# Kernel optimization log

Measured on AMD Instinct MI355X. Metric: run time of the kernel, lower is better.

Reference implementation:

```python
import jax, jax.numpy as jnp
import numpy as np

B, N, D = 4, 2048, 1024
DC = 256
E = 8            # n_experts
TOPK = 2
EXP = 4
HID = EXP * D
CAPF = 1.25
T = B * N
CAP = int(CAPF * TOPK * T / E)  # static expert capacity (2560)
EPS = 1e-5


def _transition_adaln(x, cond, mask, Wada, bada, W1, b1, W2, b2):
    # adaLN-modulated gated MLP expert: x [..., D], cond [..., DC], mask [...]
    ada = cond @ Wada + bada                      # [..., 3D]
    shift, scale, gate = jnp.split(ada, 3, axis=-1)
    mu = jnp.mean(x, axis=-1, keepdims=True)
    var = jnp.mean(jnp.square(x - mu), axis=-1, keepdims=True)
    h = (x - mu) * jax.lax.rsqrt(var + EPS)       # LayerNorm, no affine
    h = h * (1.0 + scale) + shift
    h = jax.nn.gelu(h @ W1 + b1) @ W2 + b2
    return gate * h * mask[..., None]


def setup_inputs() -> dict:
    key = jax.random.key(0)
    ks = jax.random.split(key, 16)
    s = lambda k, shp, f: jax.random.normal(k, shp, jnp.float32) * f
    return {
        "x": s(ks[0], (B, N, D), 1.0),
        "cond": s(ks[1], (B, N, DC), 1.0),
        "mask": jnp.ones((B, N), jnp.float32),
        "Wg": s(ks[2], (D, E - 1), 0.02),
        # shared expert
        "Wada_s": s(ks[3], (DC, 3 * D), 0.02),
        "bada_s": jnp.zeros((3 * D,), jnp.float32),
        "W1_s": s(ks[4], (D, HID), 0.02),
        "b1_s": jnp.zeros((HID,), jnp.float32),
        "W2_s": s(ks[5], (HID, D), 0.02),
        "b2_s": jnp.zeros((D,), jnp.float32),
        # routed experts (stacked over E)
        "Wada_e": s(ks[6], (E, DC, 3 * D), 0.02),
        "bada_e": jnp.zeros((E, 3 * D), jnp.float32),
        "W1_e": s(ks[7], (E, D, HID), 0.02),
        "b1_e": jnp.zeros((E, HID), jnp.float32),
        "W2_e": s(ks[8], (E, HID, D), 0.02),
        "b2_e": jnp.zeros((E, D), jnp.float32),
    }


def reference(x, cond, mask, Wg, Wada_s, bada_s, W1_s, b1_s, W2_s, b2_s,
              Wada_e, bada_e, W1_e, b1_e, W2_e, b2_e):
    xf = x.reshape(T, D)
    cf = cond.reshape(T, DC)
    mf = mask.reshape(T)

    # --- router: softmax over E-1 experts, top-k, normalized weights ---
    scores = jax.nn.softmax(xf @ Wg, axis=-1)              # [T, E-1]
    w, idx = jax.lax.top_k(scores, TOPK)                   # [T, K]
    w = w / jnp.sum(w, axis=-1, keepdims=True)

    flat_e = idx.reshape(-1)                               # [T*K] expert ids
    flat_w = w.reshape(-1)

    # --- indices_and_bins: stable sort by expert, histogram, cumsum ---
    order = jnp.argsort(flat_e, stable=True)               # [T*K]
    tpe = jnp.bincount(flat_e, length=E)                   # tokens per expert
    starts = jnp.cumsum(tpe) - tpe                         # exclusive cumsum

    # --- binned gather into [E, CAP] slots (overflow dropped, pad zeros) ---
    slot = jnp.arange(CAP)
    pos = starts[:, None] + slot[None, :]                  # [E, CAP]
    valid = slot[None, :] < tpe[:, None]                   # [E, CAP]
    pos_c = jnp.clip(pos, 0, T * TOPK - 1)
    sidx = order[pos_c]                                    # sorted flat index
    tok = sidx // TOPK                                     # source token id
    vf = valid.astype(x.dtype)
    xg = xf[tok] * vf[..., None]                           # [E, CAP, D]
    cg = cf[tok] * vf[..., None]                           # [E, CAP, DC]
    mg = mf[tok] * vf                                      # [E, CAP]

    # --- per-expert grouped compute (vmapped over E) ---
    y = jax.vmap(_transition_adaln)(xg, cg, mg, Wada_e, bada_e,
                                    W1_e, b1_e, W2_e, b2_e)  # [E, CAP, D]

    # --- binned scatter with expert weights ---
    w_sel = flat_w[sidx] * vf                              # [E, CAP]
    contrib = (y * w_sel[..., None]).reshape(E * CAP, D)
    moe = jnp.zeros((T, D), x.dtype).at[tok.reshape(-1)].add(contrib)
    moe = moe.reshape(B, N, D)

    # --- shared expert + normalized combine ---
    x_shared = _transition_adaln(x, cond, mask, Wada_s, bada_s,
                                 W1_s, b1_s, W2_s, b2_s)
    return (x_shared + moe * TOPK) / (TOPK + 1)
```

## Files before the change

kernel.cpp:

```cpp
#include <hip/hip_runtime.h>
#include <cstdint>

#define B_    4
#define N_    2048
#define D_    1024
#define DC_   256
#define E_    8
#define NE    7
#define HID_  4096
#define T_    8192
#define CAP_  2560
#define TP_   16384

typedef unsigned short us;

__device__ __forceinline__ float b2f(us h) {
    unsigned u = ((unsigned)h) << 16; float f; __builtin_memcpy(&f, &u, 4); return f;
}
__device__ __forceinline__ us f2b(float f) {
    unsigned u; __builtin_memcpy(&u, &f, 4);
    unsigned r = (u + 0x7fffu + ((u >> 16) & 1u)) >> 16;
    return (us)r;
}

using short8 = __attribute__((ext_vector_type(8))) short;
using f32x4  = __attribute__((ext_vector_type(4))) float;

typedef __attribute__((address_space(1))) void GASV;
typedef __attribute__((address_space(3))) void LASV;
__device__ __forceinline__ void gld16(const void* g, void* l) {
    __builtin_amdgcn_global_load_lds((GASV*)g, (LASV*)l, 16, 0, 0);
}

__global__ void sentinel_kernel(float* out) { out[0] = 12345.0f; }

__global__ __launch_bounds__(256) void router_ln_kernel(
    const float* __restrict__ x, const float* __restrict__ Wg,
    int* __restrict__ flat_e, float* __restrict__ flat_w, us* __restrict__ lnb)
{
    __shared__ float sWg[D_ * NE];
    for (int i = threadIdx.x; i < D_ * NE; i += 256) sWg[i] = Wg[i];
    __syncthreads();
    const int wave = threadIdx.x >> 6, lane = threadIdx.x & 63;
    const int t = blockIdx.x * 4 + wave;
    const float* xr = x + (size_t)t * D_;

    float v[16];
#pragma unroll
    for (int q = 0; q < 4; q++) {
        float4 f = *(const float4*)(xr + lane * 16 + q * 4);
        v[q*4+0] = f.x; v[q*4+1] = f.y; v[q*4+2] = f.z; v[q*4+3] = f.w;
    }
    float s7[NE] = {0,0,0,0,0,0,0};
    float sum = 0.f, sq = 0.f;
#pragma unroll
    for (int u = 0; u < 16; u++) {
        float xv = v[u]; int d = lane * 16 + u;
        sum += xv; sq += xv * xv;
#pragma unroll
        for (int j = 0; j < NE; j++) s7[j] += xv * sWg[d * NE + j];
    }
#pragma unroll
    for (int off = 32; off; off >>= 1) {
        sum += __shfl_xor(sum, off, 64);
        sq  += __shfl_xor(sq,  off, 64);
#pragma unroll
        for (int j = 0; j < NE; j++) s7[j] += __shfl_xor(s7[j], off, 64);
    }
    const float mu  = sum * (1.f / D_);
    const float var = sq * (1.f / D_) - mu * mu;
    const float rs  = rsqrtf(var + 1e-5f);

    us* lr = lnb + (size_t)t * D_ + lane * 16;
#pragma unroll
    for (int half = 0; half < 2; half++) {
        union { us h[8]; uint4 u4; } p;
#pragma unroll
        for (int u = 0; u < 8; u++) p.h[u] = f2b((v[half*8+u] - mu) * rs);
        *(uint4*)(lr + half * 8) = p.u4;
    }
    if (lane == 0) {
        float m = s7[0];
#pragma unroll
        for (int j = 1; j < NE; j++) m = fmaxf(m, s7[j]);
        float ex[NE];
#pragma unroll
        for (int j = 0; j < NE; j++) ex[j] = __expf(s7[j] - m);
        int i1 = 0;
#pragma unroll
        for (int j = 1; j < NE; j++) if (ex[j] > ex[i1]) i1 = j;
        int i2 = (i1 == 0) ? 1 : 0;
#pragma unroll
        for (int j = 0; j < NE; j++) if (j != i1 && ex[j] > ex[i2]) i2 = j;
        float wA = ex[i1], wB = ex[i2], iw = 1.f / (wA + wB);
        flat_e[t*2]   = i1; flat_e[t*2+1] = i2;
        flat_w[t*2]   = wA * iw; flat_w[t*2+1] = wB * iw;
    }
}

__global__ __launch_bounds__(256) void binning_kernel(
    const int* __restrict__ flat_e, int* __restrict__ bin_idx,
    int* __restrict__ dest_slot, int* __restrict__ n_e)
{
    __shared__ int hist[NE][257];
    const int t = threadIdx.x;
    const int base = t * 64;
    int cnt[NE] = {0,0,0,0,0,0,0};
    for (int i = 0; i < 64; i++) {
        int fe = flat_e[base + i];
#pragma unroll
        for (int e = 0; e < NE; e++) cnt[e] += (fe == e);
    }
#pragma unroll
    for (int e = 0; e < NE; e++) hist[e][t] = cnt[e];
    __syncthreads();
    if (t < NE) {
        int run = 0;
        for (int i = 0; i < 256; i++) { int c = hist[t][i]; hist[t][i] = run; run += c; }
        n_e[t] = run < CAP_ ? run : CAP_;
    }
    __syncthreads();
    for (int i = t; i < NE * CAP_; i += 256) bin_idx[i] = -1;
    __syncthreads();
    int ofs[NE];
#pragma unroll
    for (int e = 0; e < NE; e++) ofs[e] = hist[e][t];
    for (int i = 0; i < 64; i++) {
        int idx = base + i;
        int fe = flat_e[idx];
        int r = 0;
#pragma unroll
        for (int e = 0; e < NE; e++) if (fe == e) r = ofs[e]++;
        int slot = (r < CAP_) ? (fe * CAP_ + r) : -1;
        dest_slot[idx] = slot;
        if (slot >= 0) bin_idx[slot] = idx;
    }
}

__global__ void cvt_bf16_kernel(const float* __restrict__ in, us* __restrict__ out, long n) {
    long i = ((long)blockIdx.x * 256 + threadIdx.x) * 4;
    if (i >= n) return;
    float4 f = *(const float4*)(in + i);
    union { us h[4]; uint2 u; } p;
    p.h[0] = f2b(f.x); p.h[1] = f2b(f.y); p.h[2] = f2b(f.z); p.h[3] = f2b(f.w);
    *(uint2*)(out + i) = p.u;
}

__global__ __launch_bounds__(256) void convT_kernel(
    const float* __restrict__ W, us* __restrict__ WT, int K, int N, long sW, long sWT)
{
    const float* Wp = W + (size_t)blockIdx.z * sW;
    us* WTp = WT + (size_t)blockIdx.z * sWT;
    __shared__ us tl[32][33];
    const int k0 = blockIdx.y * 32, n0 = blockIdx.x * 32;
    const int tx = threadIdx.x & 31, ty = threadIdx.x >> 5;
#pragma unroll
    for (int r = ty; r < 32; r += 8)
        tl[r][tx] = f2b(Wp[(size_t)(k0 + r) * N + n0 + tx]);
    __syncthreads();
#pragma unroll
    for (int r = ty; r < 32; r += 8)
        WTp[(size_t)(n0 + r) * K + k0 + tx] = tl[tx][r];
}

__global__ __launch_bounds__(256) void gather_cond_kernel(
    const us* __restrict__ cond_bf, const int* __restrict__ bin_idx, us* __restrict__ cond_g)
{
    const int row = blockIdx.x * 4 + (threadIdx.x >> 6);
    const int lane = threadIdx.x & 63;
    const int pi = bin_idx[row];
    uint2 val = {0u, 0u};
    if (pi >= 0) val = *(const uint2*)(cond_bf + (size_t)(pi >> 1) * DC_ + lane * 4);
    *(uint2*)(cond_g + (size_t)row * DC_ + lane * 4) = val;
}

struct GArgs {
    const us* A; const us* BT; const float* bias;
    us* out0; us* out1; us* out2;
    const us* gateP; const float* maskP; float* outF;
    int M, N, K, ldOut;
    long sA_e, sBT_e, sBias_e, sOut_e;
    const int* n_e;
    int epi;
};

__global__ __launch_bounds__(256) void gemm_bt(GArgs g) {
    const int e = blockIdx.z;
    int rows = g.M;
    if (g.n_e) { int ne = g.n_e[e]; if (ne < rows) rows = ne; }
    const int mbase = blockIdx.y * 128;
    if (mbase >= rows) return;
    const int nbase = blockIdx.x * 128;
    const us* A  = g.A  + (size_t)e * g.sA_e;
    const us* BT = g.BT + (size_t)e * g.sBT_e;
    const int K = g.K;

    __shared__ __align__(16) us sA[128 * 32];
    __shared__ __align__(16) us sB[128 * 32];

    const int tid = threadIdx.x;
    const int wave = tid >> 6, lane = tid & 63;
    const int wm = wave >> 1, wn = wave & 1;
    const int lrow = lane & 15, lq = lane >> 4;
    const int r0 = lane >> 2;
    const int cb = (lane & 3) * 8;

    const size_t aOff0 = (size_t)(mbase + wave * 16 + r0) * K + cb;
    const size_t aOff1 = aOff0 + (size_t)64 * K;
    const size_t bOff0 = (size_t)(nbase + wave * 16 + r0) * K + cb;
    const size_t bOff1 = bOff0 + (size_t)64 * K;

    f32x4 acc[4][4];
#pragma unroll
    for (int i = 0; i < 4; i++)
#pragma unroll
        for (int j = 0; j < 4; j++) acc[i][j] = (f32x4)0.0f;

    for (int k0 = 0; k0 < K; k0 += 32) {
        gld16(A + aOff0 + k0, &sA[wave * 512]);
        gld16(A + aOff1 + k0, &sA[(wave + 4) * 512]);
        gld16(BT + bOff0 + k0, &sB[wave * 512]);
        gld16(BT + bOff1 + k0, &sB[(wave + 4) * 512]);
        __syncthreads();
        short8 af[4], bf[4];
#pragma unroll
        for (int i = 0; i < 4; i++) {
            af[i] = *(const short8*)&sA[(wm * 64 + i * 16 + lrow) * 32 + lq * 8];
            bf[i] = *(const short8*)&sB[(wn * 64 + i * 16 + lrow) * 32 + lq * 8];
        }
#pragma unroll
        for (int i = 0; i < 4; i++)
#pragma unroll
            for (int j = 0; j < 4; j++)
                acc[i][j] = __builtin_amdgcn_mfma_f32_16x16x32_bf16(af[i], bf[j], acc[i][j], 0, 0, 0);
        __syncthreads();
    }

    const float* bias = g.bias + (size_t)e * g.sBias_e;
    float bv[4];
#pragma unroll
    for (int j = 0; j < 4; j++) bv[j] = bias[nbase + wn * 64 + j * 16 + lrow];

    if (g.epi == 0) {
        const int seg = nbase >> 10;
        us* ob = (seg == 0) ? g.out0 : (seg == 1) ? g.out1 : g.out2;
        ob += (size_t)e * g.sOut_e;
        const int coll = nbase - (seg << 10) + wn * 64 + lrow;
#pragma unroll
        for (int i = 0; i < 4; i++)
#pragma unroll
            for (int r = 0; r < 4; r++) {
                int row = mbase + wm * 64 + i * 16 + lq * 4 + r;
#pragma unroll
                for (int j = 0; j < 4; j++)
                    ob[(size_t)row * 1024 + coll + j * 16] = f2b(acc[i][j][r] + bv[j]);
            }
    } else if (g.epi == 1) {
        us* ob = g.out0 + (size_t)e * g.sOut_e;
#pragma unroll
        for (int i = 0; i < 4; i++)
#pragma unroll
            for (int r = 0; r < 4; r++) {
                int row = mbase + wm * 64 + i * 16 + lq * 4 + r;
#pragma unroll
                for (int j = 0; j < 4; j++) {
                    float v = acc[i][j][r] + bv[j];
                    float u = 0.7978845608028654f * (v + 0.044715f * v * v * v);
                    float exu = __expf(2.f * u);
                    float th = 1.f - 2.f / (exu + 1.f);
                    ob[(size_t)row * g.ldOut + nbase + wn * 64 + j * 16 + lrow] = f2b(0.5f * v * (1.f + th));
                }
            }
    } else if (g.epi == 2) {
        us* ob = g.out0 + (size_t)e * g.sOut_e;
#pragma unroll
        for (int i = 0; i < 4; i++)
#pragma unroll
            for (int r = 0; r < 4; r++) {
                int row = mbase + wm * 64 + i * 16 + lq * 4 + r;
#pragma unroll
                for (int j = 0; j < 4; j++)
                    ob[(size_t)row * g.ldOut + nbase + wn * 64 + j * 16 + lrow] = f2b(acc[i][j][r] + bv[j]);
            }
    } else {
        float* ob = g.outF;
#pragma unroll
        for (int i = 0; i < 4; i++)
#pragma unroll
            for (int r = 0; r < 4; r++) {
                int row = mbase + wm * 64 + i * 16 + lq * 4 + r;
                float mrow = g.maskP[row] * (1.f / 3.f);
#pragma unroll
                for (int j = 0; j < 4; j++) {
                    int col = nbase + wn * 64 + j * 16 + lrow;
                    float v = acc[i][j][r] + bv[j];
                    ob[(size_t)row * 1024 + col] = v * b2f(g.gateP[(size_t)row * 1024 + col]) * mrow;
                }
            }
    }
}

__global__ void modulate_s_kernel(const us* __restrict__ lnb, const us* __restrict__ shift,
                                  const us* __restrict__ scale, us* __restrict__ hmod)
{
    size_t i = ((size_t)blockIdx.x * 256 + threadIdx.x) * 4;
    uint2 l  = *(const uint2*)(lnb + i);
    uint2 sh = *(const uint2*)(shift + i);
    uint2 sc = *(const uint2*)(scale + i);
    const us* lp = (const us*)&l; const us* shp = (const us*)&sh; const us* scp = (const us*)&sc;
    union { us h[4]; uint2 u; } o;
#pragma unroll
    for (int u = 0; u < 4; u++)
        o.h[u] = f2b(b2f(lp[u]) * (1.f + b2f(scp[u])) + b2f(shp[u]));
    *(uint2*)(hmod + i) = o.u;
}

__global__ void modulate_g_kernel(const us* __restrict__ lnb, const us* __restrict__ shift_g,
                                  const us* __restrict__ scale_g, const int* __restrict__ bin_idx,
                                  us* __restrict__ hmod_g)
{
    const int slot = blockIdx.x;
    const int d = threadIdx.x * 4;
    const int pi = bin_idx[slot];
    float lv[4] = {0.f, 0.f, 0.f, 0.f};
    if (pi >= 0) {
        uint2 l = *(const uint2*)(lnb + (size_t)(pi >> 1) * D_ + d);
        const us* lp = (const us*)&l;
#pragma unroll
        for (int u = 0; u < 4; u++) lv[u] = b2f(lp[u]);
    }
    const size_t off = (size_t)slot * 1024 + d;
    uint2 sh = *(const uint2*)(shift_g + off);
    uint2 sc = *(const uint2*)(scale_g + off);
    const us* shp = (const us*)&sh; const us* scp = (const us*)&sc;
    union { us h[4]; uint2 u; } o;
#pragma unroll
    for (int u = 0; u < 4; u++)
        o.h[u] = f2b(lv[u] * (1.f + b2f(scp[u])) + b2f(shp[u]));
    *(uint2*)(hmod_g + off) = o.u;
}

__global__ void combine_kernel(const us* __restrict__ y_g, const us* __restrict__ gate_g,
                               const int* __restrict__ dest_slot, const float* __restrict__ flat_w,
                               const float* __restrict__ maskp, float* __restrict__ out)
{
    const int t = blockIdx.x;
    const int d = threadIdx.x * 4;
    const size_t o = (size_t)t * D_ + d;
    float acc[4] = {0.f, 0.f, 0.f, 0.f};
    const int s0 = dest_slot[2*t], s1 = dest_slot[2*t+1];
    const float w0 = flat_w[2*t] * (2.f / 3.f), w1 = flat_w[2*t+1] * (2.f / 3.f);
    if (s0 >= 0) {
        uint2 yg = *(const uint2*)(y_g + (size_t)s0 * D_ + d);
        uint2 gg = *(const uint2*)(gate_g + (size_t)s0 * D_ + d);
        const us* yp = (const us*)&yg; const us* gp = (const us*)&gg;
#pragma unroll
        for (int u = 0; u < 4; u++) acc[u] += w0 * b2f(gp[u]) * b2f(yp[u]);
    }
    if (s1 >= 0) {
        uint2 yg = *(const uint2*)(y_g + (size_t)s1 * D_ + d);
        uint2 gg = *(const uint2*)(gate_g + (size_t)s1 * D_ + d);
        const us* yp = (const us*)&yg; const us* gp = (const us*)&gg;
#pragma unroll
        for (int u = 0; u < 4; u++) acc[u] += w1 * b2f(gp[u]) * b2f(yp[u]);
    }
    const float mk = maskp[t];
    float4 cur = *(float4*)(out + o);
    cur.x += acc[0] * mk; cur.y += acc[1] * mk;
    cur.z += acc[2] * mk; cur.w += acc[3] * mk;
    *(float4*)(out + o) = cur;
}

extern "C" void kernel_launch(void* const* d_in, const int* in_sizes, int n_in,
                              void* d_out, int out_size, void* d_ws, size_t ws_size,
                              hipStream_t stream)
{
    const float* x      = (const float*)d_in[0];
    const float* cond   = (const float*)d_in[1];
    const float* maskp  = (const float*)d_in[2];
    const float* Wg     = (const float*)d_in[3];
    const float* Wada_s = (const float*)d_in[4];
    const float* bada_s = (const float*)d_in[5];
    const float* W1_s   = (const float*)d_in[6];
    const float* b1_s   = (const float*)d_in[7];
    const float* W2_s   = (const float*)d_in[8];
    const float* b2_s   = (const float*)d_in[9];
    const float* Wada_e = (const float*)d_in[10];
    const float* bada_e = (const float*)d_in[11];
    const float* W1_e   = (const float*)d_in[12];
    const float* b1_e   = (const float*)d_in[13];
    const float* W2_e   = (const float*)d_in[14];
    const float* b2_e   = (const float*)d_in[15];
    (void)in_sizes; (void)n_in; (void)out_size;
    float* out = (float*)d_out;

    char* p = (char*)d_ws;
    size_t off = 0;
    auto carve = [&](size_t bytes) -> void* {
        void* r = p + off; off = (off + bytes + 255) & ~(size_t)255; return r;
    };
    int*   flat_e   = (int*)carve((size_t)TP_ * 4);
    float* flat_w   = (float*)carve((size_t)TP_ * 4);
    int*   bin_idx  = (int*)carve((size_t)NE * CAP_ * 4);
    int*   dest_slot= (int*)carve((size_t)TP_ * 4);
    int*   d_ne     = (int*)carve(256);
    us*    cond_bf  = (us*)carve((size_t)T_ * DC_ * 2);
    us*    lnb      = (us*)carve((size_t)T_ * D_ * 2);
    us*    gate_s   = (us*)carve((size_t)T_ * D_ * 2);
    us*    gate_g   = (us*)carve((size_t)NE * CAP_ * D_ * 2);
    us*    y_g      = (us*)carve((size_t)NE * CAP_ * D_ * 2);

    char* A = p + off;
    const size_t ARENA_SZ = 103809024;
    us* hmod_s  = (us*)(A);
    us* wt_s    = (us*)(A + 16777216);
    us* t1_s    = (us*)(A + 25165824);
    us* shift_s = (us*)(A + 25165824);
    us* scale_s = (us*)(A + 41943040);
    us* hmod_gb = (us*)(A);
    us* wt_b    = (us*)(A + 15728640);
    us* t1_gb   = (us*)(A + 40894464);
    us* shift_gb= (us*)(A + 40894464);
    us* scale_gb= (us*)(A + 40894464 + 15728640);
    us* cond_gb = (us*)(A + 40894464 + 31457280);

    if (off + ARENA_SZ > ws_size) {
        sentinel_kernel<<<1, 1, 0, stream>>>(out);
        return;
    }

    router_ln_kernel<<<T_ / 4, 256, 0, stream>>>(x, Wg, flat_e, flat_w, lnb);
    binning_kernel<<<1, 256, 0, stream>>>(flat_e, bin_idx, dest_slot, d_ne);
    cvt_bf16_kernel<<<(T_ * DC_) / 1024, 256, 0, stream>>>(cond, cond_bf, (long)T_ * DC_);

    GArgs a;
    a.gateP = nullptr; a.maskP = nullptr; a.outF = nullptr;

    convT_kernel<<<dim3(96, 8, 1), 256, 0, stream>>>(Wada_s, wt_s, DC_, 3072, 0, 0);
    a.A = cond_bf; a.BT = wt_s; a.bias = bada_s;
    a.out0 = shift_s; a.out1 = scale_s; a.out2 = gate_s;
    a.M = T_; a.N = 3072; a.K = DC_; a.ldOut = 1024;
    a.sA_e = 0; a.sBT_e = 0; a.sBias_e = 0; a.sOut_e = 0;
    a.n_e = nullptr; a.epi = 0;
    gemm_bt<<<dim3(24, T_ / 128, 1), 256, 0, stream>>>(a);

    modulate_s_kernel<<<(T_ * D_) / 1024, 256, 0, stream>>>(lnb, shift_s, scale_s, hmod_s);

    convT_kernel<<<dim3(128, 32, 1), 256, 0, stream>>>(W1_s, wt_s, D_, HID_, 0, 0);
    a.A = hmod_s; a.BT = wt_s; a.bias = b1_s; a.out0 = t1_s;
    a.M = T_; a.N = HID_; a.K = D_; a.ldOut = HID_; a.epi = 1;
    gemm_bt<<<dim3(HID_ / 128, T_ / 128, 1), 256, 0, stream>>>(a);

    convT_kernel<<<dim3(32, 128, 1), 256, 0, stream>>>(W2_s, wt_s, HID_, D_, 0, 0);
    a.A = t1_s; a.BT = wt_s; a.bias = b2_s; a.out0 = nullptr;
    a.gateP = gate_s; a.maskP = maskp; a.outF = out;
    a.M = T_; a.N = D_; a.K = HID_; a.ldOut = D_; a.epi = 3;
    gemm_bt<<<dim3(D_ / 128, T_ / 128, 1), 256, 0, stream>>>(a);
    a.gateP = nullptr; a.maskP = nullptr; a.outF = nullptr;

    const int bstart[3] = {0, 3, 6};
    const int bcnt[3]   = {3, 3, 1};
    for (int b = 0; b < 3; b++) {
        const int eb = bstart[b], Bb = bcnt[b];
        gather_cond_kernel<<<Bb * CAP_ / 4, 256, 0, stream>>>(
            cond_bf, bin_idx + (size_t)eb * CAP_, cond_gb);

        convT_kernel<<<dim3(96, 8, Bb), 256, 0, stream>>>(
            Wada_e + (size_t)eb * DC_ * 3072, wt_b, DC_, 3072,
            (long)DC_ * 3072, (long)DC_ * 3072);
        a.A = cond_gb; a.BT = wt_b; a.bias = bada_e + (size_t)eb * 3072;
        a.out0 = shift_gb; a.out1 = scale_gb;
        a.out2 = gate_g + (size_t)eb * CAP_ * 1024;
        a.M = CAP_; a.N = 3072; a.K = DC_; a.ldOut = 1024;
        a.sA_e = (long)CAP_ * DC_; a.sBT_e = (long)3072 * DC_;
        a.sBias_e = 3072; a.sOut_e = (long)CAP_ * 1024;
        a.n_e = d_ne + eb; a.epi = 0;
        gemm_bt<<<dim3(24, CAP_ / 128, Bb), 256, 0, stream>>>(a);

        modulate_g_kernel<<<Bb * CAP_, 256, 0, stream>>>(
            lnb, shift_gb, scale_gb, bin_idx + (size_t)eb * CAP_, hmod_gb);

        convT_kernel<<<dim3(128, 32, Bb), 256, 0, stream>>>(
            W1_e + (size_t)eb * D_ * HID_, wt_b, D_, HID_,
            (long)D_ * HID_, (long)D_ * HID_);
        a.A = hmod_gb; a.BT = wt_b; a.bias = b1_e + (size_t)eb * HID_; a.out0 = t1_gb;
        a.M = CAP_; a.N = HID_; a.K = D_; a.ldOut = HID_;
        a.sA_e = (long)CAP_ * D_; a.sBT_e = (long)HID_ * D_;
        a.sBias_e = HID_; a.sOut_e = (long)CAP_ * HID_;
        a.epi = 1;
        gemm_bt<<<dim3(HID_ / 128, CAP_ / 128, Bb), 256, 0, stream>>>(a);

        convT_kernel<<<dim3(32, 128, Bb), 256, 0, stream>>>(
            W2_e + (size_t)eb * HID_ * D_, wt_b, HID_, D_,
            (long)HID_ * D_, (long)HID_ * D_);
        a.A = t1_gb; a.BT = wt_b; a.bias = b2_e + (size_t)eb * D_;
        a.out0 = y_g + (size_t)eb * CAP_ * 1024;
        a.M = CAP_; a.N = D_; a.K = HID_; a.ldOut = D_;
        a.sA_e = (long)CAP_ * HID_; a.sBT_e = (long)D_ * HID_;
        a.sBias_e = D_; a.sOut_e = (long)CAP_ * 1024;
        a.epi = 2;
        gemm_bt<<<dim3(D_ / 128, CAP_ / 128, Bb), 256, 0, stream>>>(a);
    }

    combine_kernel<<<T_, 256, 0, stream>>>(y_g, gate_g, dest_slot, flat_w, maskp, out);
}
```

Baseline: 1.412 ms.

## Widen GEMM K-tile with swizzled LDS, templatize epilogues, vectorize transpose, parallel-scan binning

```diff
diff --git a/kernel.cpp b/kernel.cpp
--- a/kernel.cpp
+++ b/kernel.cpp
@@ -103,6 +103,7 @@
     int* __restrict__ dest_slot, int* __restrict__ n_e)
 {
     __shared__ int hist[NE][257];
+    __shared__ int sc[2][256];
     const int t = threadIdx.x;
     const int base = t * 64;
     int cnt[NE] = {0,0,0,0,0,0,0};
@@ -114,12 +115,21 @@
 #pragma unroll
     for (int e = 0; e < NE; e++) hist[e][t] = cnt[e];
     __syncthreads();
-    if (t < NE) {
-        int run = 0;
-        for (int i = 0; i < 256; i++) { int c = hist[t][i]; hist[t][i] = run; run += c; }
-        n_e[t] = run < CAP_ ? run : CAP_;
-    }
-    __syncthreads();
+    for (int e = 0; e < NE; e++) {
+        sc[0][t] = hist[e][t];
+        __syncthreads();
+        int src = 0;
+        for (int o = 1; o < 256; o <<= 1) {
+            int v = sc[src][t] + ((t >= o) ? sc[src][t - o] : 0);
+            sc[src ^ 1][t] = v;
+            __syncthreads();
+            src ^= 1;
+        }
+        int incl = sc[src][t];
+        hist[e][t] = incl - cnt[e];
+        if (t == 255) n_e[e] = incl < CAP_ ? incl : CAP_;
+        __syncthreads();
+    }
     for (int i = t; i < NE * CAP_; i += 256) bin_idx[i] = -1;
     __syncthreads();
     int ofs[NE];
@@ -151,16 +161,27 @@
 {
     const float* Wp = W + (size_t)blockIdx.z * sW;
     us* WTp = WT + (size_t)blockIdx.z * sWT;
-    __shared__ us tl[32][33];
-    const int k0 = blockIdx.y * 32, n0 = blockIdx.x * 32;
-    const int tx = threadIdx.x & 31, ty = threadIdx.x >> 5;
-#pragma unroll
-    for (int r = ty; r < 32; r += 8)
-        tl[r][tx] = f2b(Wp[(size_t)(k0 + r) * N + n0 + tx]);
+    __shared__ us tl[64][72];
+    const int k0 = blockIdx.y * 64, n0 = blockIdx.x * 64;
+    const int lr = threadIdx.x >> 4;
+    const int lc = threadIdx.x & 15;
+#pragma unroll
+    for (int p = 0; p < 4; p++) {
+        int r = p * 16 + lr;
+        float4 f = *(const float4*)(Wp + (size_t)(k0 + r) * N + n0 + lc * 4);
+        tl[lc*4+0][r] = f2b(f.x);
+        tl[lc*4+1][r] = f2b(f.y);
+        tl[lc*4+2][r] = f2b(f.z);
+        tl[lc*4+3][r] = f2b(f.w);
+    }
     __syncthreads();
-#pragma unroll
-    for (int r = ty; r < 32; r += 8)
-        WTp[(size_t)(n0 + r) * K + k0 + tx] = tl[tx][r];
+    const int nr = threadIdx.x >> 2, kc = (threadIdx.x & 3) * 16;
+    union { us h[16]; uint4 u4[2]; } pk;
+#pragma unroll
+    for (int u = 0; u < 16; u++) pk.h[u] = tl[nr][kc + u];
+    us* dst = WTp + (size_t)(n0 + nr) * K + k0 + kc;
+    *(uint4*)(dst) = pk.u4[0];
+    *(uint4*)(dst + 8) = pk.u4[1];
 }
 
 __global__ __launch_bounds__(256) void gather_cond_kernel(
@@ -181,58 +202,71 @@
     int M, N, K, ldOut;
     long sA_e, sBT_e, sBias_e, sOut_e;
     const int* n_e;
-    int epi;
 };
 
+template<int TN, int EPI>
 __global__ __launch_bounds__(256) void gemm_bt(GArgs g) {
     const int e = blockIdx.z;
     int rows = g.M;
     if (g.n_e) { int ne = g.n_e[e]; if (ne < rows) rows = ne; }
     const int mbase = blockIdx.y * 128;
     if (mbase >= rows) return;
-    const int nbase = blockIdx.x * 128;
-    const us* A  = g.A  + (size_t)e * g.sA_e;
-    const us* BT = g.BT + (size_t)e * g.sBT_e;
+    const int nbase = blockIdx.x * TN;
+    const us* Ap = g.A  + (size_t)e * g.sA_e;
+    const us* BTp = g.BT + (size_t)e * g.sBT_e;
     const int K = g.K;
 
-    __shared__ __align__(16) us sA[128 * 32];
-    __shared__ __align__(16) us sB[128 * 32];
+    constexpr int MI = (TN == 128) ? 4 : 2;
+    __shared__ __align__(16) us sA[128 * 64];
+    __shared__ __align__(16) us sB[TN * 64];
 
     const int tid = threadIdx.x;
     const int wave = tid >> 6, lane = tid & 63;
-    const int wm = wave >> 1, wn = wave & 1;
+    const int wm = (TN == 128) ? (wave >> 1) : wave;
+    const int wn = (TN == 128) ? (wave & 1) : 0;
     const int lrow = lane & 15, lq = lane >> 4;
-    const int r0 = lane >> 2;
-    const int cb = (lane & 3) * 8;
-
-    const size_t aOff0 = (size_t)(mbase + wave * 16 + r0) * K + cb;
-    const size_t aOff1 = aOff0 + (size_t)64 * K;
-    const size_t bOff0 = (size_t)(nbase + wave * 16 + r0) * K + cb;
-    const size_t bOff1 = bOff0 + (size_t)64 * K;
-
-    f32x4 acc[4][4];
-#pragma unroll
-    for (int i = 0; i < 4; i++)
+    const int rl = lane >> 3;
+    const int cs = (lane & 7) ^ rl;
+
+    f32x4 acc[MI][4];
+#pragma unroll
+    for (int i = 0; i < MI; i++)
 #pragma unroll
         for (int j = 0; j < 4; j++) acc[i][j] = (f32x4)0.0f;
 
-    for (int k0 = 0; k0 < K; k0 += 32) {
-        gld16(A + aOff0 + k0, &sA[wave * 512]);
-        gld16(A + aOff1 + k0, &sA[(wave + 4) * 512]);
-        gld16(BT + bOff0 + k0, &sB[wave * 512]);
-        gld16(BT + bOff1 + k0, &sB[(wave + 4) * 512]);
+    for (int k0 = 0; k0 < K; k0 += 64) {
+#pragma unroll
+        for (int q = 0; q < 4; q++) {
+            int row = wave * 32 + q * 8 + rl;
+            gld16(Ap + (size_t)(mbase + row) * K + k0 + cs * 8, &sA[(wave * 32 + q * 8) * 64]);
+        }
+#pragma unroll
+        for (int q = 0; q < TN / 32; q++) {
+            int row = wave * (TN / 4) + q * 8 + rl;
+            gld16(BTp + (size_t)(nbase + row) * K + k0 + cs * 8, &sB[(wave * (TN / 4) + q * 8) * 64]);
+        }
         __syncthreads();
-        short8 af[4], bf[4];
-#pragma unroll
-        for (int i = 0; i < 4; i++) {
-            af[i] = *(const short8*)&sA[(wm * 64 + i * 16 + lrow) * 32 + lq * 8];
-            bf[i] = *(const short8*)&sB[(wn * 64 + i * 16 + lrow) * 32 + lq * 8];
+#pragma unroll
+        for (int step = 0; step < 2; step++) {
+            short8 af[MI], bf[4];
+#pragma unroll
+            for (int i = 0; i < MI; i++) {
+                int r = wm * (MI * 16) + i * 16 + lrow;
+                int slot = (step * 4 + lq) ^ (r & 7);
+                af[i] = *(const short8*)&sA[r * 64 + slot * 8];
+            }
+#pragma unroll
+            for (int j = 0; j < 4; j++) {
+                int r = wn * 64 + j * 16 + lrow;
+                int slot = (step * 4 + lq) ^ (r & 7);
+                bf[j] = *(const short8*)&sB[r * 64 + slot * 8];
+            }
+#pragma unroll
+            for (int i = 0; i < MI; i++)
+#pragma unroll
+                for (int j = 0; j < 4; j++)
+                    acc[i][j] = __builtin_amdgcn_mfma_f32_16x16x32_bf16(af[i], bf[j], acc[i][j], 0, 0, 0);
         }
-#pragma unroll
-        for (int i = 0; i < 4; i++)
-#pragma unroll
-            for (int j = 0; j < 4; j++)
-                acc[i][j] = __builtin_amdgcn_mfma_f32_16x16x32_bf16(af[i], bf[j], acc[i][j], 0, 0, 0);
         __syncthreads();
     }
 
@@ -241,27 +275,27 @@
 #pragma unroll
     for (int j = 0; j < 4; j++) bv[j] = bias[nbase + wn * 64 + j * 16 + lrow];
 
-    if (g.epi == 0) {
+    if constexpr (EPI == 0) {
         const int seg = nbase >> 10;
         us* ob = (seg == 0) ? g.out0 : (seg == 1) ? g.out1 : g.out2;
         ob += (size_t)e * g.sOut_e;
         const int coll = nbase - (seg << 10) + wn * 64 + lrow;
 #pragma unroll
-        for (int i = 0; i < 4; i++)
+        for (int i = 0; i < MI; i++)
 #pragma unroll
             for (int r = 0; r < 4; r++) {
-                int row = mbase + wm * 64 + i * 16 + lq * 4 + r;
+                int row = mbase + wm * (MI * 16) + i * 16 + lq * 4 + r;
 #pragma unroll
                 for (int j = 0; j < 4; j++)
                     ob[(size_t)row * 1024 + coll + j * 16] = f2b(acc[i][j][r] + bv[j]);
             }
-    } else if (g.epi == 1) {
+    } else if constexpr (EPI == 1) {
         us* ob = g.out0 + (size_t)e * g.sOut_e;
 #pragma unroll
-        for (int i = 0; i < 4; i++)
+        for (int i = 0; i < MI; i++)
 #pragma unroll
             for (int r = 0; r < 4; r++) {
-                int row = mbase + wm * 64 + i * 16 + lq * 4 + r;
+                int row = mbase + wm * (MI * 16) + i * 16 + lq * 4 + r;
 #pragma unroll
                 for (int j = 0; j < 4; j++) {
                     float v = acc[i][j][r] + bv[j];
@@ -271,13 +305,13 @@
                     ob[(size_t)row * g.ldOut + nbase + wn * 64 + j * 16 + lrow] = f2b(0.5f * v * (1.f + th));
                 }
             }
-    } else if (g.epi == 2) {
+    } else if constexpr (EPI == 2) {
         us* ob = g.out0 + (size_t)e * g.sOut_e;
 #pragma unroll
-        for (int i = 0; i < 4; i++)
+        for (int i = 0; i < MI; i++)
 #pragma unroll
             for (int r = 0; r < 4; r++) {
-                int row = mbase + wm * 64 + i * 16 + lq * 4 + r;
+                int row = mbase + wm * (MI * 16) + i * 16 + lq * 4 + r;
 #pragma unroll
                 for (int j = 0; j < 4; j++)
                     ob[(size_t)row * g.ldOut + nbase + wn * 64 + j * 16 + lrow] = f2b(acc[i][j][r] + bv[j]);
@@ -285,10 +319,10 @@
     } else {
         float* ob = g.outF;
 #pragma unroll
-        for (int i = 0; i < 4; i++)
+        for (int i = 0; i < MI; i++)
 #pragma unroll
             for (int r = 0; r < 4; r++) {
-                int row = mbase + wm * 64 + i * 16 + lq * 4 + r;
+                int row = mbase + wm * (MI * 16) + i * 16 + lq * 4 + r;
                 float mrow = g.maskP[row] * (1.f / 3.f);
 #pragma unroll
                 for (int j = 0; j < 4; j++) {
@@ -436,26 +470,26 @@
     GArgs a;
     a.gateP = nullptr; a.maskP = nullptr; a.outF = nullptr;
 
-    convT_kernel<<<dim3(96, 8, 1), 256, 0, stream>>>(Wada_s, wt_s, DC_, 3072, 0, 0);
+    convT_kernel<<<dim3(48, 4, 1), 256, 0, stream>>>(Wada_s, wt_s, DC_, 3072, 0, 0);
     a.A = cond_bf; a.BT = wt_s; a.bias = bada_s;
     a.out0 = shift_s; a.out1 = scale_s; a.out2 = gate_s;
     a.M = T_; a.N = 3072; a.K = DC_; a.ldOut = 1024;
     a.sA_e = 0; a.sBT_e = 0; a.sBias_e = 0; a.sOut_e = 0;
-    a.n_e = nullptr; a.epi = 0;
-    gemm_bt<<<dim3(24, T_ / 128, 1), 256, 0, stream>>>(a);
+    a.n_e = nullptr;
+    gemm_bt<128, 0><<<dim3(24, T_ / 128, 1), 256, 0, stream>>>(a);
 
     modulate_s_kernel<<<(T_ * D_) / 1024, 256, 0, stream>>>(lnb, shift_s, scale_s, hmod_s);
 
-    convT_kernel<<<dim3(128, 32, 1), 256, 0, stream>>>(W1_s, wt_s, D_, HID_, 0, 0);
+    convT_kernel<<<dim3(64, 16, 1), 256, 0, stream>>>(W1_s, wt_s, D_, HID_, 0, 0);
     a.A = hmod_s; a.BT = wt_s; a.bias = b1_s; a.out0 = t1_s;
-    a.M = T_; a.N = HID_; a.K = D_; a.ldOut = HID_; a.epi = 1;
-    gemm_bt<<<dim3(HID_ / 128, T_ / 128, 1), 256, 0, stream>>>(a);
-
-    convT_kernel<<<dim3(32, 128, 1), 256, 0, stream>>>(W2_s, wt_s, HID_, D_, 0, 0);
+    a.M = T_; a.N = HID_; a.K = D_; a.ldOut = HID_;
+    gemm_bt<128, 1><<<dim3(HID_ / 128, T_ / 128, 1), 256, 0, stream>>>(a);
+
+    convT_kernel<<<dim3(16, 64, 1), 256, 0, stream>>>(W2_s, wt_s, HID_, D_, 0, 0);
     a.A = t1_s; a.BT = wt_s; a.bias = b2_s; a.out0 = nullptr;
     a.gateP = gate_s; a.maskP = maskp; a.outF = out;
-    a.M = T_; a.N = D_; a.K = HID_; a.ldOut = D_; a.epi = 3;
-    gemm_bt<<<dim3(D_ / 128, T_ / 128, 1), 256, 0, stream>>>(a);
+    a.M = T_; a.N = D_; a.K = HID_; a.ldOut = D_;
+    gemm_bt<64, 3><<<dim3(D_ / 64, T_ / 128, 1), 256, 0, stream>>>(a);
     a.gateP = nullptr; a.maskP = nullptr; a.outF = nullptr;
 
     const int bstart[3] = {0, 3, 6};
@@ -465,7 +499,7 @@
         gather_cond_kernel<<<Bb * CAP_ / 4, 256, 0, stream>>>(
             cond_bf, bin_idx + (size_t)eb * CAP_, cond_gb);
 
-        convT_kernel<<<dim3(96, 8, Bb), 256, 0, stream>>>(
+        convT_kernel<<<dim3(48, 4, Bb), 256, 0, stream>>>(
             Wada_e + (size_t)eb * DC_ * 3072, wt_b, DC_, 3072,
             (long)DC_ * 3072, (long)DC_ * 3072);
         a.A = cond_gb; a.BT = wt_b; a.bias = bada_e + (size_t)eb * 3072;
@@ -474,23 +508,22 @@
         a.M = CAP_; a.N = 3072; a.K = DC_; a.ldOut = 1024;
         a.sA_e = (long)CAP_ * DC_; a.sBT_e = (long)3072 * DC_;
         a.sBias_e = 3072; a.sOut_e = (long)CAP_ * 1024;
-        a.n_e = d_ne + eb; a.epi = 0;
-        gemm_bt<<<dim3(24, CAP_ / 128, Bb), 256, 0, stream>>>(a);
+        a.n_e = d_ne + eb;
+        gemm_bt<128, 0><<<dim3(24, CAP_ / 128, Bb), 256, 0, stream>>>(a);
 
         modulate_g_kernel<<<Bb * CAP_, 256, 0, stream>>>(
             lnb, shift_gb, scale_gb, bin_idx + (size_t)eb * CAP_, hmod_gb);
 
-        convT_kernel<<<dim3(128, 32, Bb), 256, 0, stream>>>(
+        convT_kernel<<<dim3(64, 16, Bb), 256, 0, stream>>>(
             W1_e + (size_t)eb * D_ * HID_, wt_b, D_, HID_,
             (long)D_ * HID_, (long)D_ * HID_);
         a.A = hmod_gb; a.BT = wt_b; a.bias = b1_e + (size_t)eb * HID_; a.out0 = t1_gb;
         a.M = CAP_; a.N = HID_; a.K = D_; a.ldOut = HID_;
         a.sA_e = (long)CAP_ * D_; a.sBT_e = (long)HID_ * D_;
         a.sBias_e = HID_; a.sOut_e = (long)CAP_ * HID_;
-        a.epi = 1;
-        gemm_bt<<<dim3(HID_ / 128, CAP_ / 128, Bb), 256, 0, stream>>>(a);
-
-        convT_kernel<<<dim3(32, 128, Bb), 256, 0, stream>>>(
+        gemm_bt<128, 1><<<dim3(HID_ / 128, CAP_ / 128, Bb), 256, 0, stream>>>(a);
+
+        convT_kernel<<<dim3(16, 64, Bb), 256, 0, stream>>>(
             W2_e + (size_t)eb * HID_ * D_, wt_b, HID_, D_,
             (long)HID_ * D_, (long)HID_ * D_);
         a.A = t1_gb; a.BT = wt_b; a.bias = b2_e + (size_t)eb * D_;
@@ -498,8 +531,7 @@
         a.M = CAP_; a.N = D_; a.K = HID_; a.ldOut = D_;
         a.sA_e = (long)CAP_ * HID_; a.sBT_e = (long)D_ * HID_;
         a.sBias_e = D_; a.sOut_e = (long)CAP_ * 1024;
-        a.epi = 2;
-        gemm_bt<<<dim3(D_ / 128, CAP_ / 128, Bb), 256, 0, stream>>>(a);
+        gemm_bt<64, 2><<<dim3(D_ / 64, CAP_ / 128, Bb), 256, 0, stream>>>(a);
     }
 
     combine_kernel<<<T_, 256, 0, stream>>>(y_g, gate_g, dest_slot, flat_w, maskp, out);
```

After: 1.210 ms. 14.3% less time.
